# Kernel tuning notes

Hardware: AMD Instinct MI355X
Metric: run time of the kernel (lower is better)

The kernel has to match this reference:

```python
import jax, jax.numpy as jnp
import numpy as np
import math

CHUNK = 128


def setup_inputs() -> dict:
    key = jax.random.key(0)
    ks = jax.random.split(key, 12)
    B, S, H, D = 2, 4096, 1024, 2048  # D = hidden_dim * expansion_factor
    std = 0.02
    inp = {
        "hidden_states": jax.random.normal(ks[0], (B, S, H), jnp.float32),
        "Wq": jax.random.normal(ks[1], (H, D), jnp.float32) * std,
        "bq": jnp.zeros((D,), jnp.float32),
        "Wk": jax.random.normal(ks[2], (H, D), jnp.float32) * std,
        "bk": jnp.zeros((D,), jnp.float32),
        "Wv": jax.random.normal(ks[3], (H, D), jnp.float32) * std,
        "bv": jnp.zeros((D,), jnp.float32),
        "Wg": jax.random.normal(ks[4], (H, D), jnp.float32) * std,
        "bg": jnp.zeros((D,), jnp.float32),
        "Wo": jax.random.normal(ks[5], (D, H), jnp.float32) * std,
        "bo": jnp.zeros((H,), jnp.float32),
    }
    return inp


def reference(hidden_states, Wq, bq, Wk, bk, Wv, bv, Wg, bg, Wo, bo):
    B, S, H = hidden_states.shape
    D = Wq.shape[1]
    cs = CHUNK
    nC = S // cs  # seq_len chosen as multiple of chunk_size (no padding path)

    q = hidden_states @ Wq + bq
    k = hidden_states @ Wk + bk
    v = hidden_states @ Wv + bv
    gate = jax.nn.sigmoid(hidden_states @ Wg + bg)

    qc = q.reshape(B, nC, cs, D)
    kc = k.reshape(B, nC, cs, D)
    vc = v.reshape(B, nC, cs, D)
    gc = gate.reshape(B, nC, cs, D)

    # intra-chunk causal softmax attention (vectorized over all chunks)
    scale = 1.0 / math.sqrt(D)
    attn = jnp.einsum('bncd,bnkd->bnck', qc, kc) * scale  # [B,nC,cs,cs]
    causal = jnp.tril(jnp.ones((cs, cs), bool))
    attn = jnp.where(causal, attn, -jnp.inf)
    attn = jax.nn.softmax(attn, axis=-1)
    local = jnp.einsum('bnck,bnkd->bncd', attn, vc)

    # inter-chunk linear-attention state accumulation:
    # cross_i = q_i @ sum_{j<i} K_j^T V_j  (sequential scan over chunks)
    def step(state, xs):
        qi, ki, vi = xs  # each [B,cs,D]
        cross = jnp.einsum('bcd,bde->bce', qi, state)
        state = state + jnp.einsum('bcd,bce->bde', ki, vi)
        return state, cross

    state0 = jnp.zeros((B, D, D), hidden_states.dtype)
    _, cross = jax.lax.scan(
        step, state0,
        (qc.transpose(1, 0, 2, 3), kc.transpose(1, 0, 2, 3), vc.transpose(1, 0, 2, 3)))
    cross = cross.transpose(1, 0, 2, 3)  # [B,nC,cs,D]

    out = (local + cross) * gc
    out = out.reshape(B, S, D)
    return out @ Wo + bo
```

## Files before the change

kernel.cpp:

```cpp
#include <hip/hip_runtime.h>
#include <hip/hip_bf16.h>
#include <math.h>


typedef __bf16 bf16_t;
typedef __bf16 bf16x8 __attribute__((ext_vector_type(8)));
typedef __bf16 bf16x4 __attribute__((ext_vector_type(4)));
typedef float f32x4 __attribute__((ext_vector_type(4)));

#define NB_ 2
#define SEQ 4096
#define HID 1024
#define DD 2048
#define BS 8192

__device__ __forceinline__ void async16(const void* g, void* l) {
  __builtin_amdgcn_global_load_lds(
      (const __attribute__((address_space(1))) void*)g,
      (__attribute__((address_space(3))) void*)l, 16, 0, 0);
}

#define VMW0 asm volatile("s_waitcnt vmcnt(0)" ::: "memory")
#define BARR __builtin_amdgcn_s_barrier()
#define FEN asm volatile("" ::: "memory")

template <int WM, int WN>
__device__ __forceinline__ void coreK32(const bf16_t* __restrict__ A, int lda,
                                        const bf16_t* __restrict__ B, int ldb, int nt,
                                        bf16_t* lds, f32x4 (&acc)[4][4]) {
  constexpr int T = WM * WN * 64;
  constexpr int AE = WM * 64 * 32;
  constexpr int BE = WN * 64 * 32;
  constexpr int BUF = AE + BE;
  constexpr int NISS = BUF / (T * 8);
  const int t = threadIdx.x;
  const int lane = t & 63, w = t >> 6;
  const int wm = w / WN, wn = w % WN;
  const int lr = lane & 15, lg = lane >> 4;

  int aOff[4], bOff[4];
#pragma unroll
  for (int f = 0; f < 4; ++f) {
    int ra = wm * 64 + f * 16 + lr;
    aOff[f] = ra * 32 + (((lg + (ra >> 1)) & 3) << 3);
    int rb = wn * 64 + f * 16 + lr;
    bOff[f] = AE + rb * 32 + (((lg + (rb >> 1)) & 3) << 3);
  }
  int src[NISS];
#pragma unroll
  for (int q = 0; q < NISS; ++q) {
    constexpr int ebase0 = 0;
    int e = q * T * 8 + t * 8;
    bool isB = (q * T * 8) >= AE;
    int e2 = isB ? e - AE : e;
    int r = e2 >> 5;
    int g = (((e2 >> 3) & 3) - (r >> 1)) & 3;
    src[q] = r * (isB ? ldb : lda) + g * 8;
    (void)ebase0;
  }
#pragma unroll
  for (int m = 0; m < 4; ++m)
#pragma unroll
    for (int n = 0; n < 4; ++n) acc[m][n] = (f32x4){0.f, 0.f, 0.f, 0.f};

  {
    bf16_t* buf0 = lds;
#pragma unroll
    for (int q = 0; q < NISS; ++q) {
      bool isB = (q * T * 8) >= AE;
      async16((isB ? B : A) + src[q], buf0 + q * T * 8 + t * 8);
    }
  }
  VMW0; BARR; FEN;

  for (int tt = 0; tt < nt; ++tt) {
    bf16_t* cur = lds + (tt & 1) * BUF;
    bf16_t* nxt = lds + ((tt + 1) & 1) * BUF;
    const int kn = (tt + 1 < nt ? tt + 1 : 0) << 5;
#pragma unroll
    for (int q = 0; q < NISS; ++q) {
      bool isB = (q * T * 8) >= AE;
      async16((isB ? B : A) + kn + src[q], nxt + q * T * 8 + t * 8);
    }
    bf16x8 af[4], bv[4];
#pragma unroll
    for (int f = 0; f < 4; ++f) af[f] = *reinterpret_cast<const bf16x8*>(&cur[aOff[f]]);
#pragma unroll
    for (int f = 0; f < 4; ++f) bv[f] = *reinterpret_cast<const bf16x8*>(&cur[bOff[f]]);
    __builtin_amdgcn_s_setprio(1);
#pragma unroll
    for (int mf = 0; mf < 4; ++mf)
#pragma unroll
      for (int nf = 0; nf < 4; ++nf)
        acc[mf][nf] =
            __builtin_amdgcn_mfma_f32_16x16x32_bf16(af[mf], bv[nf], acc[mf][nf], 0, 0, 0);
    __builtin_amdgcn_s_setprio(0);
    VMW0; BARR; FEN;
  }
}

__global__ void k_cvt(const float4* __restrict__ in, bf16x4* __restrict__ out, int n4) {
  int i = blockIdx.x * blockDim.x + threadIdx.x;
  if (i < n4) {
    float4 v = in[i];
    bf16x4 o;
    o[0] = (bf16_t)v.x; o[1] = (bf16_t)v.y; o[2] = (bf16_t)v.z; o[3] = (bf16_t)v.w;
    out[i] = o;
  }
}

__global__ void k_tconv(const float* __restrict__ in, bf16_t* __restrict__ out,
                        int R, int C) {
  __shared__ bf16_t tile[64][65];
  int bc = blockIdx.x, br = blockIdx.y;
  int t = threadIdx.x;
  int c = t & 63, r0 = t >> 6;
#pragma unroll
  for (int rr = 0; rr < 64; rr += 4) {
    int r = rr + r0;
    tile[r][c] = (bf16_t)in[(long)(br * 64 + r) * C + bc * 64 + c];
  }
  __syncthreads();
#pragma unroll
  for (int rr = 0; rr < 64; rr += 4) {
    int r = rr + r0;
    out[(long)(bc * 64 + r) * R + br * 64 + c] = tile[c][r];
  }
}

__global__ __launch_bounds__(512, 4) void k_gemm_qkvg(
    const bf16_t* __restrict__ hsb, const bf16_t* __restrict__ Wt4,
    const float* __restrict__ bq, const float* __restrict__ bk,
    const float* __restrict__ bv, const float* __restrict__ bg,
    bf16_t* __restrict__ out, bf16_t* __restrict__ Vt) {
  extern __shared__ bf16_t lds[];
  const int SP = 136;
  int i = blockIdx.x;
  int xcd = i & 7, g = i >> 3;
  int mb = g >> 3;
  int nb = xcd * 8 + (g & 7);
  f32x4 acc[4][4];
  coreK32<4, 2>(hsb + (long)mb * 256 * HID, HID, Wt4 + (long)nb * 128 * HID, HID,
                HID / 32, lds, acc);
  const int t = threadIdx.x, lane = t & 63, w = t >> 6;
  const int wm = w >> 1, wn = w & 1, lr = lane & 15, lg = lane >> 4;
  int z = nb >> 4;
  const float* bias = z == 0 ? bq : z == 1 ? bk : z == 2 ? bv : bg;
  int colT = (nb & 15) * 128;
  float b4[4];
#pragma unroll
  for (int nf = 0; nf < 4; ++nf) b4[nf] = bias[colT + wn * 64 + nf * 16 + lr];
#pragma unroll
  for (int mf = 0; mf < 4; ++mf)
#pragma unroll
    for (int reg = 0; reg < 4; ++reg) {
      int lrow = wm * 64 + mf * 16 + lg * 4 + reg;
#pragma unroll
      for (int nf = 0; nf < 4; ++nf) {
        float v = acc[mf][nf][reg] + b4[nf];
        if (z == 3) v = 1.f / (1.f + __expf(-v));
        lds[lrow * SP + wn * 64 + nf * 16 + lr] = (bf16_t)v;
      }
    }
  __syncthreads();
  if (z != 2) {
    bf16_t* O = out + (long)z * BS * DD + (long)mb * 256 * DD + colT;
#pragma unroll
    for (int it = 0; it < 8; ++it) {
      int s = it * 512 + t;
      int row = s >> 4, sg = s & 15;
      bf16x8 v = *reinterpret_cast<const bf16x8*>(&lds[row * SP + sg * 8]);
      *reinterpret_cast<bf16x8*>(&O[(long)row * DD + sg * 8]) = v;
    }
  } else {
    int bz = mb >> 4, smb = mb & 15;
    bf16_t* Vd = Vt + ((long)bz * DD + colT) * SEQ + smb * 256;
#pragma unroll
    for (int it = 0; it < 8; ++it) {
      int d = (t >> 3) + (it & 1) * 64;
      int s8 = (t & 7) * 8 + (it >> 1) * 64;
      bf16x8 v;
#pragma unroll
      for (int j = 0; j < 8; ++j) v[j] = lds[(s8 + j) * SP + d];
      *reinterpret_cast<bf16x8*>(&Vd[(long)d * SEQ + s8]) = v;
    }
  }
}

__global__ __launch_bounds__(256, 4) void k_pair(const bf16_t* __restrict__ Q,
                                                 const bf16_t* __restrict__ Kb,
                                                 bf16_t* __restrict__ P) {
  extern __shared__ bf16_t lds[];
  const int SP = 136;
  int p = blockIdx.x, b = blockIdx.y;
  int c = 0, base = 0;
  while (base + c + 1 <= p) { base += c + 1; ++c; }
  int jt = p - base;
  f32x4 acc[4][4];
  coreK32<2, 2>(Q + ((long)b * SEQ + (long)c * 128) * DD, DD,
                Kb + ((long)b * SEQ + (long)jt * 128) * DD, DD, DD / 32, lds, acc);
  const int t = threadIdx.x, lane = t & 63, w = t >> 6;
  const int wm = w >> 1, wn = w & 1, lr = lane & 15, lg = lane >> 4;
  bf16_t* Pt = P + ((long)b * SEQ + (long)c * 128) * (long)SEQ + (long)jt * 128;
  const bool diag = (jt == c);
  const float scale = 0.02209708691207961f;
#pragma unroll
  for (int mf = 0; mf < 4; ++mf)
#pragma unroll
    for (int reg = 0; reg < 4; ++reg) {
      int row = wm * 64 + mf * 16 + lg * 4 + reg;
#pragma unroll
      for (int nf = 0; nf < 4; ++nf) {
        int col = wn * 64 + nf * 16 + lr;
        float v = acc[mf][nf][reg];
        if (diag) v = (col <= row) ? v * scale : -1e30f;
        lds[row * SP + col] = (bf16_t)v;
      }
    }
  __syncthreads();
  if (diag) {
    if (t < 128) {
      int r = t;
      bf16_t* rowp = lds + r * SP;
      float mx = -1e30f;
      for (int cc = 0; cc <= r; ++cc) mx = fmaxf(mx, (float)rowp[cc]);
      float ssum = 0.f;
      for (int cc = 0; cc <= r; ++cc) ssum += __expf((float)rowp[cc] - mx);
      float inv = 1.f / ssum;
      for (int cc = 0; cc < 128; ++cc) {
        float v = (cc <= r) ? __expf((float)rowp[cc] - mx) * inv : 0.f;
        rowp[cc] = (bf16_t)v;
      }
    }
    __syncthreads();
  }
#pragma unroll
  for (int it = 0; it < 8; ++it) {
    int s = it * 256 + t;
    int row = s >> 4, sg = s & 15;
    bf16x8 v = *reinterpret_cast<const bf16x8*>(&lds[row * SP + sg * 8]);
    *reinterpret_cast<bf16x8*>(&Pt[(long)row * SEQ + sg * 8]) = v;
  }
  if (diag && !(c & 1)) {
    bf16x8 zv = {};
#pragma unroll
    for (int it = 0; it < 8; ++it) {
      int s = it * 256 + t;
      int row = s >> 4, sg = s & 15;
      *reinterpret_cast<bf16x8*>(&Pt[(long)row * SEQ + 128 + sg * 8]) = zv;
    }
  }
}

__global__ __launch_bounds__(512, 4) void k_gemm2(const bf16_t* __restrict__ P,
                                                  const bf16_t* __restrict__ Vt,
                                                  const bf16_t* __restrict__ G,
                                                  bf16_t* __restrict__ OutPre) {
  extern __shared__ bf16_t lds[];
  const int SP = 136;
  int bid = blockIdx.x;
  int ip = 15 - (bid >> 5);
  int r2 = bid & 31;
  int nb = r2 >> 1, b2 = r2 & 1;
  f32x4 acc[4][4];
  coreK32<4, 2>(P + ((long)b2 * SEQ + (long)ip * 256) * (long)SEQ, SEQ,
                Vt + (long)b2 * DD * SEQ + (long)nb * 128 * SEQ, SEQ, (ip + 1) * 8,
                lds, acc);
  const int t = threadIdx.x, lane = t & 63, w = t >> 6;
  const int wm = w >> 1, wn = w & 1, lr = lane & 15, lg = lane >> 4;
  long rowb = (long)b2 * SEQ + (long)ip * 256;
#pragma unroll
  for (int mf = 0; mf < 4; ++mf)
#pragma unroll
    for (int reg = 0; reg < 4; ++reg) {
      int lrow = wm * 64 + mf * 16 + lg * 4 + reg;
#pragma unroll
      for (int nf = 0; nf < 4; ++nf) {
        int col = wn * 64 + nf * 16 + lr;
        float gg = (float)G[(rowb + lrow) * DD + nb * 128 + col];
        lds[lrow * SP + col] = (bf16_t)(acc[mf][nf][reg] * gg);
      }
    }
  __syncthreads();
  bf16_t* O = OutPre + rowb * DD + nb * 128;
#pragma unroll
  for (int it = 0; it < 8; ++it) {
    int s = it * 512 + t;
    int row = s >> 4, sg = s & 15;
    bf16x8 v = *reinterpret_cast<const bf16x8*>(&lds[row * SP + sg * 8]);
    *reinterpret_cast<bf16x8*>(&O[(long)row * DD + sg * 8]) = v;
  }
}

__global__ __launch_bounds__(512, 4) void k_gemm3(const bf16_t* __restrict__ OutPre,
                                                  const bf16_t* __restrict__ Wot,
                                                  const float* __restrict__ bo,
                                                  float* __restrict__ out) {
  extern __shared__ bf16_t lds[];
  int mb = blockIdx.x >> 2, nb = blockIdx.x & 3;
  f32x4 acc[4][4];
  coreK32<2, 4>(OutPre + (long)mb * 128 * DD, DD, Wot + (long)nb * 256 * DD, DD,
                DD / 32, lds, acc);
  const int t = threadIdx.x, lane = t & 63, w = t >> 6;
  const int wm = w >> 2, wn = w & 3, lr = lane & 15, lg = lane >> 4;
  int colbase = nb * 256 + wn * 64;
  float b4[4];
#pragma unroll
  for (int nf = 0; nf < 4; ++nf) b4[nf] = bo[colbase + nf * 16 + lr];
#pragma unroll
  for (int mf = 0; mf < 4; ++mf)
#pragma unroll
    for (int reg = 0; reg < 4; ++reg) {
      long row = mb * 128 + wm * 64 + mf * 16 + lg * 4 + reg;
#pragma unroll
      for (int nf = 0; nf < 4; ++nf)
        out[row * HID + colbase + nf * 16 + lr] = acc[mf][nf][reg] + b4[nf];
    }
}

extern "C" void kernel_launch(void* const* d_in, const int* in_sizes, int n_in,
                              void* d_out, int out_size, void* d_ws, size_t ws_size,
                              hipStream_t stream) {
  const float* hs = (const float*)d_in[0];
  const float* Wq = (const float*)d_in[1];
  const float* bq = (const float*)d_in[2];
  const float* Wk = (const float*)d_in[3];
  const float* bk = (const float*)d_in[4];
  const float* Wv = (const float*)d_in[5];
  const float* bv = (const float*)d_in[6];
  const float* Wg = (const float*)d_in[7];
  const float* bg = (const float*)d_in[8];
  const float* Wo = (const float*)d_in[9];
  const float* bo = (const float*)d_in[10];
  float* out = (float*)d_out;

  char* ws = (char*)d_ws;
  const size_t MB = 1024 * 1024;
  bf16_t* P = (bf16_t*)(ws);
  bf16_t* hsb = (bf16_t*)(ws);
  bf16_t* Wt4 = (bf16_t*)(ws + 16 * MB);
  bf16_t* Wot = (bf16_t*)(ws + 64 * MB);
  bf16_t* QKVG = (bf16_t*)(ws + 68 * MB);
  bf16_t* Vt = (bf16_t*)(ws + 196 * MB);

  bf16_t* Qb = QKVG;
  bf16_t* Kbuf = QKVG + (long)BS * DD;
  bf16_t* Vbuf = QKVG + 2l * BS * DD;
  bf16_t* Gbuf = QKVG + 3l * BS * DD;
  bf16_t* OutPre = Vbuf;

  const int LDS_QKVG = 69632;
  const int LDS_PAIR = 34816;
  const int LDS_G2 = 69632;
  const int LDS_G3 = 49152;
  hipFuncSetAttribute((const void*)k_gemm_qkvg,
                      hipFuncAttributeMaxDynamicSharedMemorySize, LDS_QKVG);
  hipFuncSetAttribute((const void*)k_pair,
                      hipFuncAttributeMaxDynamicSharedMemorySize, LDS_PAIR);
  hipFuncSetAttribute((const void*)k_gemm2,
                      hipFuncAttributeMaxDynamicSharedMemorySize, LDS_G2);
  hipFuncSetAttribute((const void*)k_gemm3,
                      hipFuncAttributeMaxDynamicSharedMemorySize, LDS_G3);

  k_cvt<<<(BS * HID / 4 + 255) / 256, 256, 0, stream>>>((const float4*)hs,
                                                        (bf16x4*)hsb, BS * HID / 4);
  k_tconv<<<dim3(DD / 64, HID / 64), 256, 0, stream>>>(Wq, Wt4 + 0l * DD * HID, HID, DD);
  k_tconv<<<dim3(DD / 64, HID / 64), 256, 0, stream>>>(Wk, Wt4 + 1l * DD * HID, HID, DD);
  k_tconv<<<dim3(DD / 64, HID / 64), 256, 0, stream>>>(Wv, Wt4 + 2l * DD * HID, HID, DD);
  k_tconv<<<dim3(DD / 64, HID / 64), 256, 0, stream>>>(Wg, Wt4 + 3l * DD * HID, HID, DD);
  k_tconv<<<dim3(HID / 64, DD / 64), 256, 0, stream>>>(Wo, Wot, DD, HID);

  k_gemm_qkvg<<<2048, 512, LDS_QKVG, stream>>>(hsb, Wt4, bq, bk, bv, bg, QKVG, Vt);

  k_pair<<<dim3(528, 2), 256, LDS_PAIR, stream>>>(Qb, Kbuf, P);

  k_gemm2<<<512, 512, LDS_G2, stream>>>(P, Vt, Gbuf, OutPre);

  k_gemm3<<<256, 512, LDS_G3, stream>>>(OutPre, Wot, bo, out);
}
```

Baseline: 454.8 us.

## Switch all GEMMs to 256x256 tiles with K64 double-buffered split-issue core

Replaces the templated 32-deep GEMM core with a fixed 256x256 tile core that stages 64-wide K slices in two halves. It uses a new XOR swizzle and a partial vmcnt wait, so the loads for the next half-slice overlap the MFMAs on the current one. All four GEMM kernels (QKVG projection, QK pair scores, P·V, output projection) move to this tile, with fewer, larger blocks at one block per CU and 128KB LDS. Epilogues are reworked to write out in two 128-row halves. The intent is higher arithmetic intensity per LDS load and fewer blocks. The costs are lower occupancy, and wave imbalance in the triangular pair and P·V grids, where far fewer blocks are launched (272 and 256).

New measurement: 525.5 us. 15.6% more time.

```diff
diff --git a/kernel.cpp b/kernel.cpp
--- a/kernel.cpp
+++ b/kernel.cpp
@@ -13,6 +13,8 @@
 #define HID 1024
 #define DD 2048
 #define BS 8192
+#define LDS_CORE 131072
+#define SP 264
 
 __device__ __forceinline__ void async16(const void* g, void* l) {
   __builtin_amdgcn_global_load_lds(
@@ -20,83 +22,78 @@
       (__attribute__((address_space(3))) void*)l, 16, 0, 0);
 }
 
+#define VMW4 asm volatile("s_waitcnt vmcnt(4)" ::: "memory")
 #define VMW0 asm volatile("s_waitcnt vmcnt(0)" ::: "memory")
 #define BARR __builtin_amdgcn_s_barrier()
 #define FEN asm volatile("" ::: "memory")
 
-template <int WM, int WN>
-__device__ __forceinline__ void coreK32(const bf16_t* __restrict__ A, int lda,
+__device__ __forceinline__ void core256(const bf16_t* __restrict__ A, int lda,
                                         const bf16_t* __restrict__ B, int ldb, int nt,
-                                        bf16_t* lds, f32x4 (&acc)[4][4]) {
-  constexpr int T = WM * WN * 64;
-  constexpr int AE = WM * 64 * 32;
-  constexpr int BE = WN * 64 * 32;
-  constexpr int BUF = AE + BE;
-  constexpr int NISS = BUF / (T * 8);
-  const int t = threadIdx.x;
-  const int lane = t & 63, w = t >> 6;
-  const int wm = w / WN, wn = w % WN;
+                                        bf16_t* lds, f32x4 (&acc)[8][4]) {
+  constexpr int UE = 16384;
+  constexpr int BUFE = 32768;
+  const int t = threadIdx.x, lane = t & 63, w = t >> 6;
+  const int wm = w >> 2, wn = w & 3;
   const int lr = lane & 15, lg = lane >> 4;
-
-  int aOff[4], bOff[4];
-#pragma unroll
-  for (int f = 0; f < 4; ++f) {
-    int ra = wm * 64 + f * 16 + lr;
-    aOff[f] = ra * 32 + (((lg + (ra >> 1)) & 3) << 3);
-    int rb = wn * 64 + f * 16 + lr;
-    bOff[f] = AE + rb * 32 + (((lg + (rb >> 1)) & 3) << 3);
-  }
-  int src[NISS];
-#pragma unroll
-  for (int q = 0; q < NISS; ++q) {
-    constexpr int ebase0 = 0;
-    int e = q * T * 8 + t * 8;
-    bool isB = (q * T * 8) >= AE;
-    int e2 = isB ? e - AE : e;
-    int r = e2 >> 5;
-    int g = (((e2 >> 3) & 3) - (r >> 1)) & 3;
-    src[q] = r * (isB ? ldb : lda) + g * 8;
-    (void)ebase0;
-  }
-#pragma unroll
-  for (int m = 0; m < 4; ++m)
+  const int sw8 = (lg ^ (lr & 3)) * 8;
+  int aOff[8], bOff[4];
+#pragma unroll
+  for (int f = 0; f < 8; ++f) aOff[f] = (wm * 128 + f * 16 + lr) * 32 + sw8;
+#pragma unroll
+  for (int n = 0; n < 4; ++n) bOff[n] = 8192 + (wn * 64 + n * 16 + lr) * 32 + sw8;
+  const int ssl = ((t & 3) ^ ((t >> 2) & 3)) * 8;
+  const int r0 = t >> 2;
+  const int srcA0 = r0 * lda + ssl, srcA1 = (128 + r0) * lda + ssl;
+  const int srcB0 = r0 * ldb + ssl, srcB1 = (128 + r0) * ldb + ssl;
+  const int dstT = t * 8;
+
+#pragma unroll
+  for (int m = 0; m < 8; ++m)
 #pragma unroll
     for (int n = 0; n < 4; ++n) acc[m][n] = (f32x4){0.f, 0.f, 0.f, 0.f};
 
-  {
-    bf16_t* buf0 = lds;
-#pragma unroll
-    for (int q = 0; q < NISS; ++q) {
-      bool isB = (q * T * 8) >= AE;
-      async16((isB ? B : A) + src[q], buf0 + q * T * 8 + t * 8);
+#define ISSUE_UNIT(Ak, Bk, buf, h)                       \
+  {                                                      \
+    bf16_t* u_ = (buf) + (h)*UE;                         \
+    const bf16_t* a_ = (Ak) + (h)*32;                    \
+    const bf16_t* b_ = (Bk) + (h)*32;                    \
+    async16(a_ + srcA0, u_ + dstT);                      \
+    async16(a_ + srcA1, u_ + 4096 + dstT);               \
+    async16(b_ + srcB0, u_ + 8192 + dstT);               \
+    async16(b_ + srcB1, u_ + 12288 + dstT);              \
+  }
+
+  ISSUE_UNIT(A, B, lds, 0);
+  ISSUE_UNIT(A, B, lds, 1);
+
+  for (int tt = 0; tt < nt; ++tt) {
+    bf16_t* cur = lds + (tt & 1) * BUFE;
+    bf16_t* nxt = lds + ((tt + 1) & 1) * BUFE;
+    const int kb = (tt + 1 < nt ? tt + 1 : 0) << 6;
+    const bf16_t* An = A + kb;
+    const bf16_t* Bn = B + kb;
+#pragma unroll
+    for (int h = 0; h < 2; ++h) {
+      VMW4; BARR; FEN;
+      const bf16_t* u = cur + h * UE;
+      bf16x8 af[8], bv[4];
+#pragma unroll
+      for (int f = 0; f < 8; ++f) af[f] = *reinterpret_cast<const bf16x8*>(&u[aOff[f]]);
+#pragma unroll
+      for (int n = 0; n < 4; ++n) bv[n] = *reinterpret_cast<const bf16x8*>(&u[bOff[n]]);
+      ISSUE_UNIT(An, Bn, nxt, h);
+      __builtin_amdgcn_s_setprio(1);
+#pragma unroll
+      for (int mf = 0; mf < 8; ++mf)
+#pragma unroll
+        for (int nf = 0; nf < 4; ++nf)
+          acc[mf][nf] = __builtin_amdgcn_mfma_f32_16x16x32_bf16(af[mf], bv[nf],
+                                                                acc[mf][nf], 0, 0, 0);
+      __builtin_amdgcn_s_setprio(0);
     }
   }
   VMW0; BARR; FEN;
-
-  for (int tt = 0; tt < nt; ++tt) {
-    bf16_t* cur = lds + (tt & 1) * BUF;
-    bf16_t* nxt = lds + ((tt + 1) & 1) * BUF;
-    const int kn = (tt + 1 < nt ? tt + 1 : 0) << 5;
-#pragma unroll
-    for (int q = 0; q < NISS; ++q) {
-      bool isB = (q * T * 8) >= AE;
-      async16((isB ? B : A) + kn + src[q], nxt + q * T * 8 + t * 8);
-    }
-    bf16x8 af[4], bv[4];
-#pragma unroll
-    for (int f = 0; f < 4; ++f) af[f] = *reinterpret_cast<const bf16x8*>(&cur[aOff[f]]);
-#pragma unroll
-    for (int f = 0; f < 4; ++f) bv[f] = *reinterpret_cast<const bf16x8*>(&cur[bOff[f]]);
-    __builtin_amdgcn_s_setprio(1);
-#pragma unroll
-    for (int mf = 0; mf < 4; ++mf)
-#pragma unroll
-      for (int nf = 0; nf < 4; ++nf)
-        acc[mf][nf] =
-            __builtin_amdgcn_mfma_f32_16x16x32_bf16(af[mf], bv[nf], acc[mf][nf], 0, 0, 0);
-    __builtin_amdgcn_s_setprio(0);
-    VMW0; BARR; FEN;
-  }
+#undef ISSUE_UNIT
 }
 
 __global__ void k_cvt(const float4* __restrict__ in, bf16x4* __restrict__ out, int n4) {
@@ -128,179 +125,191 @@
   }
 }
 
-__global__ __launch_bounds__(512, 4) void k_gemm_qkvg(
+__global__ __launch_bounds__(512, 1) void k_gemm_qkvg(
     const bf16_t* __restrict__ hsb, const bf16_t* __restrict__ Wt4,
     const float* __restrict__ bq, const float* __restrict__ bk,
     const float* __restrict__ bv, const float* __restrict__ bg,
     bf16_t* __restrict__ out, bf16_t* __restrict__ Vt) {
   extern __shared__ bf16_t lds[];
-  const int SP = 136;
   int i = blockIdx.x;
-  int xcd = i & 7, g = i >> 3;
-  int mb = g >> 3;
-  int nb = xcd * 8 + (g & 7);
-  f32x4 acc[4][4];
-  coreK32<4, 2>(hsb + (long)mb * 256 * HID, HID, Wt4 + (long)nb * 128 * HID, HID,
-                HID / 32, lds, acc);
-  const int t = threadIdx.x, lane = t & 63, w = t >> 6;
-  const int wm = w >> 1, wn = w & 1, lr = lane & 15, lg = lane >> 4;
-  int z = nb >> 4;
+  int xcd = i & 7, j = i >> 3;
+  int nb = xcd * 4 + (j & 3);
+  int mb = j >> 2;
+  f32x4 acc[8][4];
+  core256(hsb + (long)mb * 256 * HID, HID, Wt4 + (long)nb * 256 * HID, HID,
+          HID / 64, lds, acc);
+  const int t = threadIdx.x, lane = t & 63, w = t >> 6;
+  const int wm = w >> 2, wn = w & 3, lr = lane & 15, lg = lane >> 4;
+  int z = nb >> 3;
   const float* bias = z == 0 ? bq : z == 1 ? bk : z == 2 ? bv : bg;
-  int colT = (nb & 15) * 128;
+  int colT = (nb & 7) * 256;
   float b4[4];
 #pragma unroll
   for (int nf = 0; nf < 4; ++nf) b4[nf] = bias[colT + wn * 64 + nf * 16 + lr];
 #pragma unroll
-  for (int mf = 0; mf < 4; ++mf)
-#pragma unroll
-    for (int reg = 0; reg < 4; ++reg) {
-      int lrow = wm * 64 + mf * 16 + lg * 4 + reg;
-#pragma unroll
-      for (int nf = 0; nf < 4; ++nf) {
-        float v = acc[mf][nf][reg] + b4[nf];
-        if (z == 3) v = 1.f / (1.f + __expf(-v));
-        lds[lrow * SP + wn * 64 + nf * 16 + lr] = (bf16_t)v;
+  for (int rh = 0; rh < 2; ++rh) {
+    if (wm == rh) {
+#pragma unroll
+      for (int mf = 0; mf < 8; ++mf)
+#pragma unroll
+        for (int reg = 0; reg < 4; ++reg) {
+          int lrow = mf * 16 + lg * 4 + reg;
+#pragma unroll
+          for (int nf = 0; nf < 4; ++nf) {
+            float v = acc[mf][nf][reg] + b4[nf];
+            if (z == 3) v = 1.f / (1.f + __expf(-v));
+            lds[lrow * SP + wn * 64 + nf * 16 + lr] = (bf16_t)v;
+          }
+        }
+    }
+    __syncthreads();
+    if (z != 2) {
+      bf16_t* O = out + (long)z * BS * DD + ((long)mb * 256 + rh * 128) * DD + colT;
+#pragma unroll
+      for (int it = 0; it < 8; ++it) {
+        int s = it * 512 + t;
+        int row = s >> 5, sg = s & 31;
+        bf16x8 v = *reinterpret_cast<const bf16x8*>(&lds[row * SP + sg * 8]);
+        *reinterpret_cast<bf16x8*>(&O[(long)row * DD + sg * 8]) = v;
       }
-    }
-  __syncthreads();
-  if (z != 2) {
-    bf16_t* O = out + (long)z * BS * DD + (long)mb * 256 * DD + colT;
-#pragma unroll
-    for (int it = 0; it < 8; ++it) {
-      int s = it * 512 + t;
-      int row = s >> 4, sg = s & 15;
-      bf16x8 v = *reinterpret_cast<const bf16x8*>(&lds[row * SP + sg * 8]);
-      *reinterpret_cast<bf16x8*>(&O[(long)row * DD + sg * 8]) = v;
-    }
-  } else {
-    int bz = mb >> 4, smb = mb & 15;
-    bf16_t* Vd = Vt + ((long)bz * DD + colT) * SEQ + smb * 256;
-#pragma unroll
-    for (int it = 0; it < 8; ++it) {
-      int d = (t >> 3) + (it & 1) * 64;
-      int s8 = (t & 7) * 8 + (it >> 1) * 64;
-      bf16x8 v;
-#pragma unroll
-      for (int j = 0; j < 8; ++j) v[j] = lds[(s8 + j) * SP + d];
-      *reinterpret_cast<bf16x8*>(&Vd[(long)d * SEQ + s8]) = v;
-    }
-  }
-}
-
-__global__ __launch_bounds__(256, 4) void k_pair(const bf16_t* __restrict__ Q,
+    } else {
+      int bz = mb >> 4, smb = mb & 15;
+      bf16_t* Vd = Vt + ((long)bz * DD + colT) * SEQ + smb * 256 + rh * 128;
+#pragma unroll
+      for (int it = 0; it < 8; ++it) {
+        int idx = it * 512 + t;
+        int d = idx >> 4, sg = idx & 15;
+        bf16x8 v;
+#pragma unroll
+        for (int jj = 0; jj < 8; ++jj) v[jj] = lds[(sg * 8 + jj) * SP + d];
+        *reinterpret_cast<bf16x8*>(&Vd[(long)d * SEQ + sg * 8]) = v;
+      }
+    }
+    __syncthreads();
+  }
+}
+
+__global__ __launch_bounds__(512, 1) void k_pair(const bf16_t* __restrict__ Q,
                                                  const bf16_t* __restrict__ Kb,
                                                  bf16_t* __restrict__ P) {
   extern __shared__ bf16_t lds[];
-  const int SP = 136;
   int p = blockIdx.x, b = blockIdx.y;
-  int c = 0, base = 0;
-  while (base + c + 1 <= p) { base += c + 1; ++c; }
+  int m = 0, base = 0;
+  while (base + m + 1 <= p) { base += m + 1; ++m; }
   int jt = p - base;
-  f32x4 acc[4][4];
-  coreK32<2, 2>(Q + ((long)b * SEQ + (long)c * 128) * DD, DD,
-                Kb + ((long)b * SEQ + (long)jt * 128) * DD, DD, DD / 32, lds, acc);
-  const int t = threadIdx.x, lane = t & 63, w = t >> 6;
-  const int wm = w >> 1, wn = w & 1, lr = lane & 15, lg = lane >> 4;
-  bf16_t* Pt = P + ((long)b * SEQ + (long)c * 128) * (long)SEQ + (long)jt * 128;
-  const bool diag = (jt == c);
+  f32x4 acc[8][4];
+  core256(Q + ((long)b * SEQ + (long)m * 256) * DD, DD,
+          Kb + ((long)b * SEQ + (long)jt * 256) * DD, DD, DD / 64, lds, acc);
+  const int t = threadIdx.x, lane = t & 63, w = t >> 6;
+  const int wm = w >> 2, wn = w & 3, lr = lane & 15, lg = lane >> 4;
+  const bool diag = (jt == m);
   const float scale = 0.02209708691207961f;
-#pragma unroll
-  for (int mf = 0; mf < 4; ++mf)
-#pragma unroll
-    for (int reg = 0; reg < 4; ++reg) {
-      int row = wm * 64 + mf * 16 + lg * 4 + reg;
-#pragma unroll
-      for (int nf = 0; nf < 4; ++nf) {
-        int col = wn * 64 + nf * 16 + lr;
-        float v = acc[mf][nf][reg];
-        if (diag) v = (col <= row) ? v * scale : -1e30f;
-        lds[row * SP + col] = (bf16_t)v;
+  bf16_t* Pt = P + ((long)b * SEQ + (long)m * 256) * (long)SEQ + (long)jt * 256;
+#pragma unroll
+  for (int rh = 0; rh < 2; ++rh) {
+    if (wm == rh) {
+#pragma unroll
+      for (int mf = 0; mf < 8; ++mf)
+#pragma unroll
+        for (int reg = 0; reg < 4; ++reg) {
+          int lrow = mf * 16 + lg * 4 + reg;
+#pragma unroll
+          for (int nf = 0; nf < 4; ++nf) {
+            int col = wn * 64 + nf * 16 + lr;
+            float v = acc[mf][nf][reg];
+            if (diag) {
+              int ch = col >> 7, c2 = col & 127;
+              if (ch == rh) v = (c2 <= lrow) ? v * scale : -1e30f;
+              else if (rh == 0) v = 0.f;
+            }
+            lds[lrow * SP + col] = (bf16_t)v;
+          }
+        }
+    }
+    __syncthreads();
+    if (diag) {
+      if (t < 128) {
+        bf16_t* rowp = lds + t * SP + rh * 128;
+        float mx = -1e30f;
+        for (int cc = 0; cc <= t; ++cc) mx = fmaxf(mx, (float)rowp[cc]);
+        float ssum = 0.f;
+        for (int cc = 0; cc <= t; ++cc) ssum += __expf((float)rowp[cc] - mx);
+        float inv = 1.f / ssum;
+        for (int cc = 0; cc < 128; ++cc) {
+          float v = (cc <= t) ? __expf((float)rowp[cc] - mx) * inv : 0.f;
+          rowp[cc] = (bf16_t)v;
+        }
       }
-    }
-  __syncthreads();
-  if (diag) {
-    if (t < 128) {
-      int r = t;
-      bf16_t* rowp = lds + r * SP;
-      float mx = -1e30f;
-      for (int cc = 0; cc <= r; ++cc) mx = fmaxf(mx, (float)rowp[cc]);
-      float ssum = 0.f;
-      for (int cc = 0; cc <= r; ++cc) ssum += __expf((float)rowp[cc] - mx);
-      float inv = 1.f / ssum;
-      for (int cc = 0; cc < 128; ++cc) {
-        float v = (cc <= r) ? __expf((float)rowp[cc] - mx) * inv : 0.f;
-        rowp[cc] = (bf16_t)v;
-      }
-    }
-    __syncthreads();
-  }
-#pragma unroll
-  for (int it = 0; it < 8; ++it) {
-    int s = it * 256 + t;
-    int row = s >> 4, sg = s & 15;
-    bf16x8 v = *reinterpret_cast<const bf16x8*>(&lds[row * SP + sg * 8]);
-    *reinterpret_cast<bf16x8*>(&Pt[(long)row * SEQ + sg * 8]) = v;
-  }
-  if (diag && !(c & 1)) {
-    bf16x8 zv = {};
+      __syncthreads();
+    }
+    bf16_t* Po = Pt + (long)rh * 128 * SEQ;
 #pragma unroll
     for (int it = 0; it < 8; ++it) {
-      int s = it * 256 + t;
-      int row = s >> 4, sg = s & 15;
-      *reinterpret_cast<bf16x8*>(&Pt[(long)row * SEQ + 128 + sg * 8]) = zv;
-    }
-  }
-}
-
-__global__ __launch_bounds__(512, 4) void k_gemm2(const bf16_t* __restrict__ P,
+      int s = it * 512 + t;
+      int row = s >> 5, sg = s & 31;
+      bf16x8 v = *reinterpret_cast<const bf16x8*>(&lds[row * SP + sg * 8]);
+      *reinterpret_cast<bf16x8*>(&Po[(long)row * SEQ + sg * 8]) = v;
+    }
+    __syncthreads();
+  }
+}
+
+__global__ __launch_bounds__(512, 1) void k_gemm2(const bf16_t* __restrict__ P,
                                                   const bf16_t* __restrict__ Vt,
                                                   const bf16_t* __restrict__ G,
                                                   bf16_t* __restrict__ OutPre) {
   extern __shared__ bf16_t lds[];
-  const int SP = 136;
   int bid = blockIdx.x;
-  int ip = 15 - (bid >> 5);
-  int r2 = bid & 31;
-  int nb = r2 >> 1, b2 = r2 & 1;
-  f32x4 acc[4][4];
-  coreK32<4, 2>(P + ((long)b2 * SEQ + (long)ip * 256) * (long)SEQ, SEQ,
-                Vt + (long)b2 * DD * SEQ + (long)nb * 128 * SEQ, SEQ, (ip + 1) * 8,
-                lds, acc);
-  const int t = threadIdx.x, lane = t & 63, w = t >> 6;
-  const int wm = w >> 1, wn = w & 1, lr = lane & 15, lg = lane >> 4;
+  int ip = 15 - (bid >> 4);
+  int nb = (bid >> 1) & 7, b2 = bid & 1;
+  f32x4 acc[8][4];
+  core256(P + ((long)b2 * SEQ + (long)ip * 256) * (long)SEQ, SEQ,
+          Vt + (long)b2 * DD * SEQ + (long)nb * 256 * SEQ, SEQ, (ip + 1) * 4,
+          lds, acc);
+  const int t = threadIdx.x, lane = t & 63, w = t >> 6;
+  const int wm = w >> 2, wn = w & 3, lr = lane & 15, lg = lane >> 4;
   long rowb = (long)b2 * SEQ + (long)ip * 256;
-#pragma unroll
-  for (int mf = 0; mf < 4; ++mf)
-#pragma unroll
-    for (int reg = 0; reg < 4; ++reg) {
-      int lrow = wm * 64 + mf * 16 + lg * 4 + reg;
-#pragma unroll
-      for (int nf = 0; nf < 4; ++nf) {
-        int col = wn * 64 + nf * 16 + lr;
-        float gg = (float)G[(rowb + lrow) * DD + nb * 128 + col];
-        lds[lrow * SP + col] = (bf16_t)(acc[mf][nf][reg] * gg);
-      }
-    }
-  __syncthreads();
-  bf16_t* O = OutPre + rowb * DD + nb * 128;
-#pragma unroll
-  for (int it = 0; it < 8; ++it) {
-    int s = it * 512 + t;
-    int row = s >> 4, sg = s & 15;
-    bf16x8 v = *reinterpret_cast<const bf16x8*>(&lds[row * SP + sg * 8]);
-    *reinterpret_cast<bf16x8*>(&O[(long)row * DD + sg * 8]) = v;
-  }
-}
-
-__global__ __launch_bounds__(512, 4) void k_gemm3(const bf16_t* __restrict__ OutPre,
+  int colT = nb * 256;
+#pragma unroll
+  for (int rh = 0; rh < 2; ++rh) {
+    if (wm == rh) {
+#pragma unroll
+      for (int mf = 0; mf < 8; ++mf)
+#pragma unroll
+        for (int reg = 0; reg < 4; ++reg) {
+          int lrow = mf * 16 + lg * 4 + reg;
+#pragma unroll
+          for (int nf = 0; nf < 4; ++nf)
+            lds[lrow * SP + wn * 64 + nf * 16 + lr] = (bf16_t)acc[mf][nf][reg];
+        }
+    }
+    __syncthreads();
+    bf16_t* O = OutPre + (rowb + rh * 128) * DD + colT;
+    const bf16_t* Gp = G + (rowb + rh * 128) * DD + colT;
+#pragma unroll
+    for (int it = 0; it < 8; ++it) {
+      int s = it * 512 + t;
+      int row = s >> 5, sg = s & 31;
+      bf16x8 v = *reinterpret_cast<const bf16x8*>(&lds[row * SP + sg * 8]);
+      bf16x8 gv = *reinterpret_cast<const bf16x8*>(&Gp[(long)row * DD + sg * 8]);
+      bf16x8 o;
+#pragma unroll
+      for (int jj = 0; jj < 8; ++jj) o[jj] = (bf16_t)((float)v[jj] * (float)gv[jj]);
+      *reinterpret_cast<bf16x8*>(&O[(long)row * DD + sg * 8]) = o;
+    }
+    __syncthreads();
+  }
+}
+
+__global__ __launch_bounds__(512, 1) void k_gemm3(const bf16_t* __restrict__ OutPre,
                                                   const bf16_t* __restrict__ Wot,
                                                   const float* __restrict__ bo,
                                                   float* __restrict__ out) {
   extern __shared__ bf16_t lds[];
   int mb = blockIdx.x >> 2, nb = blockIdx.x & 3;
-  f32x4 acc[4][4];
-  coreK32<2, 4>(OutPre + (long)mb * 128 * DD, DD, Wot + (long)nb * 256 * DD, DD,
-                DD / 32, lds, acc);
+  f32x4 acc[8][4];
+  core256(OutPre + (long)mb * 256 * DD, DD, Wot + (long)nb * 256 * DD, DD,
+          DD / 64, lds, acc);
   const int t = threadIdx.x, lane = t & 63, w = t >> 6;
   const int wm = w >> 2, wn = w & 3, lr = lane & 15, lg = lane >> 4;
   int colbase = nb * 256 + wn * 64;
@@ -308,10 +317,10 @@
 #pragma unroll
   for (int nf = 0; nf < 4; ++nf) b4[nf] = bo[colbase + nf * 16 + lr];
 #pragma unroll
-  for (int mf = 0; mf < 4; ++mf)
+  for (int mf = 0; mf < 8; ++mf)
 #pragma unroll
     for (int reg = 0; reg < 4; ++reg) {
-      long row = mb * 128 + wm * 64 + mf * 16 + lg * 4 + reg;
+      long row = mb * 256 + wm * 128 + mf * 16 + lg * 4 + reg;
 #pragma unroll
       for (int nf = 0; nf < 4; ++nf)
         out[row * HID + colbase + nf * 16 + lr] = acc[mf][nf][reg] + b4[nf];
@@ -349,18 +358,14 @@
   bf16_t* Gbuf = QKVG + 3l * BS * DD;
   bf16_t* OutPre = Vbuf;
 
-  const int LDS_QKVG = 69632;
-  const int LDS_PAIR = 34816;
-  const int LDS_G2 = 69632;
-  const int LDS_G3 = 49152;
   hipFuncSetAttribute((const void*)k_gemm_qkvg,
-                      hipFuncAttributeMaxDynamicSharedMemorySize, LDS_QKVG);
+                      hipFuncAttributeMaxDynamicSharedMemorySize, LDS_CORE);
   hipFuncSetAttribute((const void*)k_pair,
-                      hipFuncAttributeMaxDynamicSharedMemorySize, LDS_PAIR);
+                      hipFuncAttributeMaxDynamicSharedMemorySize, LDS_CORE);
   hipFuncSetAttribute((const void*)k_gemm2,
-                      hipFuncAttributeMaxDynamicSharedMemorySize, LDS_G2);
+                      hipFuncAttributeMaxDynamicSharedMemorySize, LDS_CORE);
   hipFuncSetAttribute((const void*)k_gemm3,
-                      hipFuncAttributeMaxDynamicSharedMemorySize, LDS_G3);
+                      hipFuncAttributeMaxDynamicSharedMemorySize, LDS_CORE);
 
   k_cvt<<<(BS * HID / 4 + 255) / 256, 256, 0, stream>>>((const float4*)hs,
                                                         (bf16x4*)hsb, BS * HID / 4);
@@ -370,11 +375,11 @@
   k_tconv<<<dim3(DD / 64, HID / 64), 256, 0, stream>>>(Wg, Wt4 + 3l * DD * HID, HID, DD);
   k_tconv<<<dim3(HID / 64, DD / 64), 256, 0, stream>>>(Wo, Wot, DD, HID);
 
-  k_gemm_qkvg<<<2048, 512, LDS_QKVG, stream>>>(hsb, Wt4, bq, bk, bv, bg, QKVG, Vt);
-
-  k_pair<<<dim3(528, 2), 256, LDS_PAIR, stream>>>(Qb, Kbuf, P);
-
-  k_gemm2<<<512, 512, LDS_G2, stream>>>(P, Vt, Gbuf, OutPre);
-
-  k_gemm3<<<256, 512, LDS_G3, stream>>>(OutPre, Wot, bo, out);
-}
+  k_gemm_qkvg<<<1024, 512, LDS_CORE, stream>>>(hsb, Wt4, bq, bk, bv, bg, QKVG, Vt);
+
+  k_pair<<<dim3(136, 2), 512, LDS_CORE, stream>>>(Qb, Kbuf, P);
+
+  k_gemm2<<<256, 512, LDS_CORE, stream>>>(P, Vt, Gbuf, OutPre);
+
+  k_gemm3<<<128, 512, LDS_CORE, stream>>>(OutPre, Wot, bo, out);
+}
```

## Triple-buffer GEMM LDS pipeline and transpose V through LDS

Applied to the files above, without the earlier changes.

Replaces the double-buffered K-loop with a three-stage LDS ring. Loads are issued two tiles ahead, and the loop waits only on the oldest outstanding batch of async global-to-LDS copies, so there is one barrier per iteration instead of a full vmcnt(0) drain. The V epilogue now writes a transposed tile into LDS so the Vt store reads contiguous 16-byte vectors instead of gathering scalar elements. The cost is more LDS per block (73728 bytes for the large GEMMs), which can reduce occupancy, and k_pair's launch bound is lowered from 4 to 3 blocks.

New measurement: 433.5 us. -4.7%, faster.

```diff
diff --git a/kernel.cpp b/kernel.cpp
--- a/kernel.cpp
+++ b/kernel.cpp
@@ -13,6 +13,8 @@
 #define HID 1024
 #define DD 2048
 #define BS 8192
+#define LDS_BIG 73728
+#define LDS_PAIR 49152
 
 __device__ __forceinline__ void async16(const void* g, void* l) {
   __builtin_amdgcn_global_load_lds(
@@ -25,13 +27,12 @@
 #define FEN asm volatile("" ::: "memory")
 
 template <int WM, int WN>
-__device__ __forceinline__ void coreK32(const bf16_t* __restrict__ A, int lda,
-                                        const bf16_t* __restrict__ B, int ldb, int nt,
-                                        bf16_t* lds, f32x4 (&acc)[4][4]) {
+__device__ __forceinline__ void coreTB(const bf16_t* __restrict__ A, int lda,
+                                       const bf16_t* __restrict__ B, int ldb, int nt,
+                                       bf16_t* lds, f32x4 (&acc)[4][4]) {
   constexpr int T = WM * WN * 64;
   constexpr int AE = WM * 64 * 32;
-  constexpr int BE = WN * 64 * 32;
-  constexpr int BUF = AE + BE;
+  constexpr int BUF = AE + WN * 64 * 32;
   constexpr int NISS = BUF / (T * 8);
   const int t = threadIdx.x;
   const int lane = t & 63, w = t >> 6;
@@ -49,44 +50,54 @@
   int src[NISS];
 #pragma unroll
   for (int q = 0; q < NISS; ++q) {
-    constexpr int ebase0 = 0;
     int e = q * T * 8 + t * 8;
     bool isB = (q * T * 8) >= AE;
     int e2 = isB ? e - AE : e;
     int r = e2 >> 5;
     int g = (((e2 >> 3) & 3) - (r >> 1)) & 3;
     src[q] = r * (isB ? ldb : lda) + g * 8;
-    (void)ebase0;
   }
 #pragma unroll
   for (int m = 0; m < 4; ++m)
 #pragma unroll
     for (int n = 0; n < 4; ++n) acc[m][n] = (f32x4){0.f, 0.f, 0.f, 0.f};
 
+#pragma unroll
+  for (int q = 0; q < NISS; ++q) {
+    bool isB = (q * T * 8) >= AE;
+    async16((isB ? B : A) + src[q], lds + q * T * 8 + t * 8);
+  }
   {
-    bf16_t* buf0 = lds;
+    const int k1 = (1 < nt ? 1 : 0) << 5;
 #pragma unroll
     for (int q = 0; q < NISS; ++q) {
       bool isB = (q * T * 8) >= AE;
-      async16((isB ? B : A) + src[q], buf0 + q * T * 8 + t * 8);
-    }
-  }
-  VMW0; BARR; FEN;
+      async16((isB ? B : A) + k1 + src[q], lds + BUF + q * T * 8 + t * 8);
+    }
+  }
 
   for (int tt = 0; tt < nt; ++tt) {
-    bf16_t* cur = lds + (tt & 1) * BUF;
-    bf16_t* nxt = lds + ((tt + 1) & 1) * BUF;
-    const int kn = (tt + 1 < nt ? tt + 1 : 0) << 5;
+    bf16_t* cur = lds + (tt % 3) * BUF;
+    bf16_t* nxt = lds + ((tt + 2) % 3) * BUF;
+    const int kn = (tt + 2 < nt ? tt + 2 : 0) << 5;
+    if constexpr (NISS == 3) {
+      asm volatile("s_waitcnt vmcnt(3)" ::: "memory");
+    } else if constexpr (NISS == 4) {
+      asm volatile("s_waitcnt vmcnt(4)" ::: "memory");
+    } else {
+      asm volatile("s_waitcnt vmcnt(0)" ::: "memory");
+    }
+    BARR; FEN;
+    bf16x8 af[4], bv[4];
+#pragma unroll
+    for (int f = 0; f < 4; ++f) af[f] = *reinterpret_cast<const bf16x8*>(&cur[aOff[f]]);
+#pragma unroll
+    for (int f = 0; f < 4; ++f) bv[f] = *reinterpret_cast<const bf16x8*>(&cur[bOff[f]]);
 #pragma unroll
     for (int q = 0; q < NISS; ++q) {
       bool isB = (q * T * 8) >= AE;
       async16((isB ? B : A) + kn + src[q], nxt + q * T * 8 + t * 8);
     }
-    bf16x8 af[4], bv[4];
-#pragma unroll
-    for (int f = 0; f < 4; ++f) af[f] = *reinterpret_cast<const bf16x8*>(&cur[aOff[f]]);
-#pragma unroll
-    for (int f = 0; f < 4; ++f) bv[f] = *reinterpret_cast<const bf16x8*>(&cur[bOff[f]]);
     __builtin_amdgcn_s_setprio(1);
 #pragma unroll
     for (int mf = 0; mf < 4; ++mf)
@@ -95,8 +106,9 @@
         acc[mf][nf] =
             __builtin_amdgcn_mfma_f32_16x16x32_bf16(af[mf], bv[nf], acc[mf][nf], 0, 0, 0);
     __builtin_amdgcn_s_setprio(0);
-    VMW0; BARR; FEN;
-  }
+  }
+  VMW0;
+  BARR; FEN;
 }
 
 __global__ void k_cvt(const float4* __restrict__ in, bf16x4* __restrict__ out, int n4) {
@@ -135,13 +147,14 @@
     bf16_t* __restrict__ out, bf16_t* __restrict__ Vt) {
   extern __shared__ bf16_t lds[];
   const int SP = 136;
+  const int SPT = 264;
   int i = blockIdx.x;
   int xcd = i & 7, g = i >> 3;
   int mb = g >> 3;
   int nb = xcd * 8 + (g & 7);
   f32x4 acc[4][4];
-  coreK32<4, 2>(hsb + (long)mb * 256 * HID, HID, Wt4 + (long)nb * 128 * HID, HID,
-                HID / 32, lds, acc);
+  coreTB<4, 2>(hsb + (long)mb * 256 * HID, HID, Wt4 + (long)nb * 128 * HID, HID,
+               HID / 32, lds, acc);
   const int t = threadIdx.x, lane = t & 63, w = t >> 6;
   const int wm = w >> 1, wn = w & 1, lr = lane & 15, lg = lane >> 4;
   int z = nb >> 4;
@@ -150,20 +163,20 @@
   float b4[4];
 #pragma unroll
   for (int nf = 0; nf < 4; ++nf) b4[nf] = bias[colT + wn * 64 + nf * 16 + lr];
-#pragma unroll
-  for (int mf = 0; mf < 4; ++mf)
-#pragma unroll
-    for (int reg = 0; reg < 4; ++reg) {
-      int lrow = wm * 64 + mf * 16 + lg * 4 + reg;
-#pragma unroll
-      for (int nf = 0; nf < 4; ++nf) {
-        float v = acc[mf][nf][reg] + b4[nf];
-        if (z == 3) v = 1.f / (1.f + __expf(-v));
-        lds[lrow * SP + wn * 64 + nf * 16 + lr] = (bf16_t)v;
-      }
-    }
-  __syncthreads();
   if (z != 2) {
+#pragma unroll
+    for (int mf = 0; mf < 4; ++mf)
+#pragma unroll
+      for (int reg = 0; reg < 4; ++reg) {
+        int lrow = wm * 64 + mf * 16 + lg * 4 + reg;
+#pragma unroll
+        for (int nf = 0; nf < 4; ++nf) {
+          float v = acc[mf][nf][reg] + b4[nf];
+          if (z == 3) v = 1.f / (1.f + __expf(-v));
+          lds[lrow * SP + wn * 64 + nf * 16 + lr] = (bf16_t)v;
+        }
+      }
+    __syncthreads();
     bf16_t* O = out + (long)z * BS * DD + (long)mb * 256 * DD + colT;
 #pragma unroll
     for (int it = 0; it < 8; ++it) {
@@ -173,21 +186,31 @@
       *reinterpret_cast<bf16x8*>(&O[(long)row * DD + sg * 8]) = v;
     }
   } else {
+#pragma unroll
+    for (int mf = 0; mf < 4; ++mf)
+#pragma unroll
+      for (int reg = 0; reg < 4; ++reg) {
+        int lrow = wm * 64 + mf * 16 + lg * 4 + reg;
+#pragma unroll
+        for (int nf = 0; nf < 4; ++nf) {
+          int d = wn * 64 + nf * 16 + lr;
+          lds[d * SPT + lrow] = (bf16_t)(acc[mf][nf][reg] + b4[nf]);
+        }
+      }
+    __syncthreads();
     int bz = mb >> 4, smb = mb & 15;
     bf16_t* Vd = Vt + ((long)bz * DD + colT) * SEQ + smb * 256;
 #pragma unroll
     for (int it = 0; it < 8; ++it) {
-      int d = (t >> 3) + (it & 1) * 64;
-      int s8 = (t & 7) * 8 + (it >> 1) * 64;
-      bf16x8 v;
-#pragma unroll
-      for (int j = 0; j < 8; ++j) v[j] = lds[(s8 + j) * SP + d];
-      *reinterpret_cast<bf16x8*>(&Vd[(long)d * SEQ + s8]) = v;
-    }
-  }
-}
-
-__global__ __launch_bounds__(256, 4) void k_pair(const bf16_t* __restrict__ Q,
+      int s = it * 512 + t;
+      int d = s >> 5, sg = s & 31;
+      bf16x8 v = *reinterpret_cast<const bf16x8*>(&lds[d * SPT + sg * 8]);
+      *reinterpret_cast<bf16x8*>(&Vd[(long)d * SEQ + sg * 8]) = v;
+    }
+  }
+}
+
+__global__ __launch_bounds__(256, 3) void k_pair(const bf16_t* __restrict__ Q,
                                                  const bf16_t* __restrict__ Kb,
                                                  bf16_t* __restrict__ P) {
   extern __shared__ bf16_t lds[];
@@ -197,8 +220,8 @@
   while (base + c + 1 <= p) { base += c + 1; ++c; }
   int jt = p - base;
   f32x4 acc[4][4];
-  coreK32<2, 2>(Q + ((long)b * SEQ + (long)c * 128) * DD, DD,
-                Kb + ((long)b * SEQ + (long)jt * 128) * DD, DD, DD / 32, lds, acc);
+  coreTB<2, 2>(Q + ((long)b * SEQ + (long)c * 128) * DD, DD,
+               Kb + ((long)b * SEQ + (long)jt * 128) * DD, DD, DD / 32, lds, acc);
   const int t = threadIdx.x, lane = t & 63, w = t >> 6;
   const int wm = w >> 1, wn = w & 1, lr = lane & 15, lg = lane >> 4;
   bf16_t* Pt = P + ((long)b * SEQ + (long)c * 128) * (long)SEQ + (long)jt * 128;
@@ -263,9 +286,9 @@
   int r2 = bid & 31;
   int nb = r2 >> 1, b2 = r2 & 1;
   f32x4 acc[4][4];
-  coreK32<4, 2>(P + ((long)b2 * SEQ + (long)ip * 256) * (long)SEQ, SEQ,
-                Vt + (long)b2 * DD * SEQ + (long)nb * 128 * SEQ, SEQ, (ip + 1) * 8,
-                lds, acc);
+  coreTB<4, 2>(P + ((long)b2 * SEQ + (long)ip * 256) * (long)SEQ, SEQ,
+               Vt + (long)b2 * DD * SEQ + (long)nb * 128 * SEQ, SEQ, (ip + 1) * 8,
+               lds, acc);
   const int t = threadIdx.x, lane = t & 63, w = t >> 6;
   const int wm = w >> 1, wn = w & 1, lr = lane & 15, lg = lane >> 4;
   long rowb = (long)b2 * SEQ + (long)ip * 256;
@@ -299,8 +322,8 @@
   extern __shared__ bf16_t lds[];
   int mb = blockIdx.x >> 2, nb = blockIdx.x & 3;
   f32x4 acc[4][4];
-  coreK32<2, 4>(OutPre + (long)mb * 128 * DD, DD, Wot + (long)nb * 256 * DD, DD,
-                DD / 32, lds, acc);
+  coreTB<2, 4>(OutPre + (long)mb * 128 * DD, DD, Wot + (long)nb * 256 * DD, DD,
+               DD / 32, lds, acc);
   const int t = threadIdx.x, lane = t & 63, w = t >> 6;
   const int wm = w >> 2, wn = w & 3, lr = lane & 15, lg = lane >> 4;
   int colbase = nb * 256 + wn * 64;
@@ -349,18 +372,14 @@
   bf16_t* Gbuf = QKVG + 3l * BS * DD;
   bf16_t* OutPre = Vbuf;
 
-  const int LDS_QKVG = 69632;
-  const int LDS_PAIR = 34816;
-  const int LDS_G2 = 69632;
-  const int LDS_G3 = 49152;
   hipFuncSetAttribute((const void*)k_gemm_qkvg,
-                      hipFuncAttributeMaxDynamicSharedMemorySize, LDS_QKVG);
+                      hipFuncAttributeMaxDynamicSharedMemorySize, LDS_BIG);
   hipFuncSetAttribute((const void*)k_pair,
                       hipFuncAttributeMaxDynamicSharedMemorySize, LDS_PAIR);
   hipFuncSetAttribute((const void*)k_gemm2,
-                      hipFuncAttributeMaxDynamicSharedMemorySize, LDS_G2);
+                      hipFuncAttributeMaxDynamicSharedMemorySize, LDS_BIG);
   hipFuncSetAttribute((const void*)k_gemm3,
-                      hipFuncAttributeMaxDynamicSharedMemorySize, LDS_G3);
+                      hipFuncAttributeMaxDynamicSharedMemorySize, LDS_BIG);
 
   k_cvt<<<(BS * HID / 4 + 255) / 256, 256, 0, stream>>>((const float4*)hs,
                                                         (bf16x4*)hsb, BS * HID / 4);
@@ -370,11 +389,11 @@
   k_tconv<<<dim3(DD / 64, HID / 64), 256, 0, stream>>>(Wg, Wt4 + 3l * DD * HID, HID, DD);
   k_tconv<<<dim3(HID / 64, DD / 64), 256, 0, stream>>>(Wo, Wot, DD, HID);
 
-  k_gemm_qkvg<<<2048, 512, LDS_QKVG, stream>>>(hsb, Wt4, bq, bk, bv, bg, QKVG, Vt);
+  k_gemm_qkvg<<<2048, 512, LDS_BIG, stream>>>(hsb, Wt4, bq, bk, bv, bg, QKVG, Vt);
 
   k_pair<<<dim3(528, 2), 256, LDS_PAIR, stream>>>(Qb, Kbuf, P);
 
-  k_gemm2<<<512, 512, LDS_G2, stream>>>(P, Vt, Gbuf, OutPre);
-
-  k_gemm3<<<256, 512, LDS_G3, stream>>>(OutPre, Wot, bo, out);
-}
+  k_gemm2<<<512, 512, LDS_BIG, stream>>>(P, Vt, Gbuf, OutPre);
+
+  k_gemm3<<<256, 512, LDS_BIG, stream>>>(OutPre, Wot, bo, out);
+}
```
